# Optimization experiments

Hardware: AMD Instinct MI355X
Metric: run time of the kernel (lower is better)

The kernel has to match this reference:

```python
import jax, jax.numpy as jnp
import numpy as np

D_MODEL = 1024
N_HEADS = 16
HEAD_DIM = D_MODEL // N_HEADS


def setup_inputs() -> dict:
    key = jax.random.key(0)
    ks = jax.random.split(key, 11)
    B, S = 4, 2048
    scale = 1.0 / np.sqrt(D_MODEL)
    inp = {
        "Q": jax.random.normal(ks[0], (B, S, D_MODEL), jnp.float32),
        "K": jax.random.normal(ks[1], (B, S, D_MODEL), jnp.float32),
        "V": jax.random.normal(ks[2], (B, S, D_MODEL), jnp.float32),
        "Wq": jax.random.normal(ks[3], (D_MODEL, D_MODEL), jnp.float32) * scale,
        "bq": jnp.zeros((D_MODEL,), jnp.float32),
        "Wk": jax.random.normal(ks[4], (D_MODEL, D_MODEL), jnp.float32) * scale,
        "bk": jnp.zeros((D_MODEL,), jnp.float32),
        "Wv": jax.random.normal(ks[5], (D_MODEL, D_MODEL), jnp.float32) * scale,
        "bv": jnp.zeros((D_MODEL,), jnp.float32),
        "Wo": jax.random.normal(ks[6], (D_MODEL, D_MODEL), jnp.float32) * scale,
        "bo": jnp.zeros((D_MODEL,), jnp.float32),
    }
    return inp


def reference(Q, K, V, Wq, bq, Wk, bk, Wv, bv, Wo, bo):
    B, S, _ = Q.shape
    # Linear projections (torch nn.Linear: x @ W.T + b)
    q = Q @ Wq.T + bq
    k = K @ Wk.T + bk
    v = V @ Wv.T + bv
    # [B, S, H, Dh] -> [B, H, S, Dh]
    q = q.reshape(B, S, N_HEADS, HEAD_DIM).transpose(0, 2, 1, 3)
    k = k.reshape(B, S, N_HEADS, HEAD_DIM).transpose(0, 2, 1, 3)
    v = v.reshape(B, S, N_HEADS, HEAD_DIM).transpose(0, 2, 1, 3)
    inv_sqrt_dh = 1.0 / np.sqrt(HEAD_DIM)
    scores = jnp.einsum("bhqd,bhkd->bhqk", q, k) * inv_sqrt_dh  # [B,H,S,S]
    attn = jax.nn.softmax(scores, axis=-1)
    out = jnp.einsum("bhqk,bhkd->bhqd", attn, v)  # [B,H,S,Dh]
    out = out.transpose(0, 2, 1, 3).reshape(B, S, D_MODEL)
    return out @ Wo.T + bo
```

## Files before the change

kernel.cpp:

```cpp
#include <hip/hip_runtime.h>
#include <hip/hip_bf16.h>
#include <stdint.h>
#include <stddef.h>


typedef __bf16 bf16_t;
typedef __bf16 bf16x4 __attribute__((ext_vector_type(4)));
typedef __bf16 bf16x8 __attribute__((ext_vector_type(8)));
typedef float f32x4 __attribute__((ext_vector_type(4)));

#define D_MODEL 1024
#define M_ROWS  8192
#define S_LEN   2048
#define N_HEADS 16
#define HEAD_DIM 64
#define GBK 32
#define NT (D_MODEL / GBK)

__device__ __forceinline__ void async_copy16(void* lds, const void* g) {
    __builtin_amdgcn_global_load_lds(
        (const __attribute__((address_space(1))) void*)g,
        (__attribute__((address_space(3))) void*)lds, 16, 0, 0);
}

__global__ __launch_bounds__(256) void conv_w(
    const float* __restrict__ s0, const float* __restrict__ s1, const float* __restrict__ s2,
    bf16_t* __restrict__ d0, bf16_t* __restrict__ d1, bf16_t* __restrict__ d2)
{
    const float* s; bf16_t* d;
    if (blockIdx.y == 0)      { s = s0; d = d0; }
    else if (blockIdx.y == 1) { s = s1; d = d1; }
    else                      { s = s2; d = d2; }
    const int i = (blockIdx.x * 256 + threadIdx.x) * 8;
    const f32x4 a = *(const f32x4*)(s + i);
    const f32x4 b = *(const f32x4*)(s + i + 4);
    bf16x8 o;
#pragma unroll
    for (int j = 0; j < 4; j++) { o[j] = (bf16_t)a[j]; o[4 + j] = (bf16_t)b[j]; }
    *(bf16x8*)(d + i) = o;
}

__global__ __launch_bounds__(256, 3) void gemm_proj(
    const float* __restrict__ A0, const bf16_t* __restrict__ W0, const float* __restrict__ b0,
    const float* __restrict__ A1, const bf16_t* __restrict__ W1, const float* __restrict__ b1,
    const float* __restrict__ A2, const bf16_t* __restrict__ W2, const float* __restrict__ b2,
    bf16_t* C0, bf16_t* C1, bf16_t* C2)
{
    const int lin = blockIdx.x + ((int)blockIdx.y << 3) + ((int)blockIdx.z << 9);
    const int nl  = (lin & 7) * 192 + (lin >> 3);
    const int z   = nl >> 9;
    const int rem = nl & 511;
    const int bm0 = (rem >> 3) * 128;
    const int bn0 = (rem & 7) * 128;

    const float* A; const bf16_t* W; const float* bias; bf16_t* C;
    if (z == 0)      { A = A0; W = W0; bias = b0; C = C0; }
    else if (z == 1) { A = A1; W = W1; bias = b1; C = C1; }
    else             { A = A2; W = W2; bias = b2; C = C2; }
    const float cs = (z == 1) ? 1.4426950408889634f : 1.0f;

    __align__(16) __shared__ bf16_t sA[2][128 * 36];
    __align__(16) __shared__ bf16_t sW[2][128 * GBK];

    const int t    = threadIdx.x;
    const int lane = t & 63;
    const int w    = t >> 6;
    const int wm   = (w & 1) * 64;
    const int wn   = (w >> 1) * 64;
    const int q4   = lane >> 4;
    const int l16  = lane & 15;

    const int srow  = t >> 1;
    const int cbase = (t & 1) * 2;
    const float* aptr = &A[(size_t)(bm0 + srow) * D_MODEL + cbase * 8];

    auto stageW = [&](int buf, int kt) {
#pragma unroll
        for (int i = 0; i < 2; i++) {
            const int cid = i * 256 + t;
            const int row = cid >> 2;
            const int cg  = (cid & 3) ^ (row & 3);
            async_copy16(&sW[buf][cid * 8],
                         &W[(size_t)(bn0 + row) * D_MODEL + kt * GBK + cg * 8]);
        }
    };

    f32x4 arA[4], arB[4];
#pragma unroll
    for (int c = 0; c < 4; c++) {
        arA[c] = *(const f32x4*)(aptr + c * 4);
        arB[c] = *(const f32x4*)(aptr + GBK + c * 4);
    }
    stageW(0, 0);

    f32x4 acc[4][4];
    const f32x4 zero4 = {0.f, 0.f, 0.f, 0.f};
#pragma unroll
    for (int i = 0; i < 4; i++)
#pragma unroll
        for (int j = 0; j < 4; j++) acc[i][j] = zero4;

    auto body = [&](int kt, int buf, f32x4 (&ar)[4]) {
        bf16x8 abf[2];
#pragma unroll
        for (int c = 0; c < 4; c++)
#pragma unroll
            for (int j = 0; j < 4; j++)
                abf[c >> 1][(c & 1) * 4 + j] = (bf16_t)ar[c][j];
#pragma unroll
        for (int hb = 0; hb < 2; hb++) {
            const int slot = (cbase + hb) ^ (srow & 3);
            *(bf16x8*)&sA[buf][srow * 36 + slot * 8] = abf[hb];
        }
        __syncthreads();
        if (kt + 2 < NT) {
            const float* ap = aptr + (size_t)(kt + 2) * GBK;
#pragma unroll
            for (int c = 0; c < 4; c++) ar[c] = *(const f32x4*)(ap + c * 4);
        }
        if (kt + 1 < NT) stageW(buf ^ 1, kt + 1);

        bf16x8 af[4], bfr[4];
#pragma unroll
        for (int i = 0; i < 4; i++) {
            const int m = wm + i * 16 + l16;
            af[i]  = *(const bf16x8*)&sA[buf][m * 36 + (q4 ^ (m & 3)) * 8];
            const int n = wn + i * 16 + l16;
            bfr[i] = *(const bf16x8*)&sW[buf][n * GBK + (q4 ^ (n & 3)) * 8];
        }
#pragma unroll
        for (int i = 0; i < 4; i++)
#pragma unroll
            for (int j = 0; j < 4; j++)
                acc[i][j] = __builtin_amdgcn_mfma_f32_16x16x32_bf16(af[i], bfr[j], acc[i][j], 0, 0, 0);
    };

    for (int kt = 0; kt < NT; kt += 2) {
        body(kt,     0, arA);
        body(kt + 1, 1, arB);
    }

    if (z != 2) {
#pragma unroll
        for (int j = 0; j < 4; j++) {
            const int col = bn0 + wn + j * 16 + l16;
            const float bj = bias[col];
#pragma unroll
            for (int i = 0; i < 4; i++) {
                const int rowb = bm0 + wm + i * 16 + q4 * 4;
#pragma unroll
                for (int r = 0; r < 4; r++)
                    C[(size_t)(rowb + r) * D_MODEL + col] = (bf16_t)((acc[i][j][r] + bj) * cs);
            }
        }
    } else {
        const int bb = bm0 >> 11;
        const int sbase = (bm0 & 2047) + wm;
#pragma unroll
        for (int j = 0; j < 4; j++) {
            const int col = bn0 + wn + j * 16 + l16;
            const float bj = bias[col];
            bf16_t* ct = C + ((size_t)bb * 1024 + col) * 2048;
#pragma unroll
            for (int i = 0; i < 4; i++) {
                const int s0 = sbase + i * 16 + q4 * 4;
                const int s0p = (s0 & ~31) | (((s0 >> 2) & 3) << 3) | (((s0 >> 4) & 1) << 2);
                bf16x4 v4;
#pragma unroll
                for (int r = 0; r < 4; r++) v4[r] = (bf16_t)(acc[i][j][r] + bj);
                *(bf16x4*)&ct[s0p] = v4;
            }
        }
    }
}

__global__ __launch_bounds__(256, 3) void gemm_out(
    const bf16_t* __restrict__ A, const bf16_t* __restrict__ W,
    const float* __restrict__ bias, float* __restrict__ C)
{
    const int lin = blockIdx.x + ((int)blockIdx.y << 3);
    const int nl  = (lin & 7) * 64 + (lin >> 3);
    const int bm0 = (nl >> 3) * 128;
    const int bn0 = (nl & 7) * 128;

    __align__(16) __shared__ bf16_t sA[2][128 * GBK];
    __align__(16) __shared__ bf16_t sW[2][128 * GBK];

    const int t    = threadIdx.x;
    const int lane = t & 63;
    const int w    = t >> 6;
    const int wm   = (w & 1) * 64;
    const int wn   = (w >> 1) * 64;
    const int q4   = lane >> 4;
    const int l16  = lane & 15;

    auto stage = [&](int buf, int kt) {
#pragma unroll
        for (int i = 0; i < 2; i++) {
            const int cid = i * 256 + t;
            const int row = cid >> 2;
            const int cg  = (cid & 3) ^ (row & 3);
            async_copy16(&sA[buf][cid * 8],
                         &A[(size_t)(bm0 + row) * D_MODEL + kt * GBK + cg * 8]);
            async_copy16(&sW[buf][cid * 8],
                         &W[(size_t)(bn0 + row) * D_MODEL + kt * GBK + cg * 8]);
        }
    };

    stage(0, 0);

    f32x4 acc[4][4];
    const f32x4 zero4 = {0.f, 0.f, 0.f, 0.f};
#pragma unroll
    for (int i = 0; i < 4; i++)
#pragma unroll
        for (int j = 0; j < 4; j++) acc[i][j] = zero4;

    for (int kt = 0; kt < NT; ++kt) {
        const int buf = kt & 1;
        __syncthreads();
        if (kt + 1 < NT) stage(buf ^ 1, kt + 1);

        bf16x8 af[4], bfr[4];
#pragma unroll
        for (int i = 0; i < 4; i++) {
            const int m = wm + i * 16 + l16;
            af[i]  = *(const bf16x8*)&sA[buf][m * GBK + (q4 ^ (m & 3)) * 8];
            const int n = wn + i * 16 + l16;
            bfr[i] = *(const bf16x8*)&sW[buf][n * GBK + (q4 ^ (n & 3)) * 8];
        }
#pragma unroll
        for (int i = 0; i < 4; i++)
#pragma unroll
            for (int j = 0; j < 4; j++)
                acc[i][j] = __builtin_amdgcn_mfma_f32_16x16x32_bf16(af[i], bfr[j], acc[i][j], 0, 0, 0);
    }

#pragma unroll
    for (int j = 0; j < 4; j++) {
        const int col = bn0 + wn + j * 16 + l16;
        const float bj = bias[col];
#pragma unroll
        for (int i = 0; i < 4; i++) {
            const int rowb = bm0 + wm + i * 16 + q4 * 4;
#pragma unroll
            for (int r = 0; r < 4; r++)
                C[(size_t)(rowb + r) * D_MODEL + col] = acc[i][j][r] + bj;
        }
    }
}

#define KVT (S_LEN / 128)

__global__ __launch_bounds__(512, 3) void attn_fused(
    const bf16_t* __restrict__ q, const bf16_t* __restrict__ k,
    const bf16_t* __restrict__ vt, bf16_t* o)
{
    __align__(16) __shared__ bf16_t sK[2][128 * 64];
    __align__(16) __shared__ bf16_t sVt[2][64 * 128];

    const int t    = threadIdx.x;
    const int lane = t & 63;
    const int w    = t >> 6;
    const int head = blockIdx.x;
    const int b    = head >> 4;
    const int h    = head & 15;
    const size_t base = (size_t)b * S_LEN * D_MODEL + (size_t)h * HEAD_DIM;
    const bf16_t* vth = vt + ((size_t)b * 1024 + h * 64) * 2048;
    const int qt0  = blockIdx.y * 256;
    const int q4   = lane >> 4;
    const int l16  = lane & 15;

    bf16x8 qf[2][2];
#pragma unroll
    for (int mg = 0; mg < 2; mg++)
#pragma unroll
        for (int kk = 0; kk < 2; kk++) {
            bf16x8 tmp = *(const bf16x8*)&q[base + (size_t)(qt0 + w * 32 + mg * 16 + l16) * D_MODEL + kk * 32 + q4 * 8];
#pragma unroll
            for (int j = 0; j < 8; j++) tmp[j] = (bf16_t)((float)tmp[j] * 0.125f);
            qf[mg][kk] = tmp;
        }

    f32x4 oacc[2][4];
    const f32x4 zero4 = {0.f, 0.f, 0.f, 0.f};
#pragma unroll
    for (int mg = 0; mg < 2; mg++)
#pragma unroll
        for (int g = 0; g < 4; g++) oacc[mg][g] = zero4;
    float lsum[2] = {0.f, 0.f};

    auto stage = [&](int bf, int kt) {
        const int key0 = kt * 128;
#pragma unroll
        for (int i = 0; i < 2; i++) {
            const int cid = i * 512 + t;
            const int row = cid >> 3;
            const int cg  = (cid & 7) ^ (row & 7);
            async_copy16(&sK[bf][cid * 8], &k[base + (size_t)(key0 + row) * D_MODEL + cg * 8]);
        }
#pragma unroll
        for (int i = 0; i < 2; i++) {
            const int cid = i * 512 + t;
            const int dh  = cid >> 4;
            const int cg  = (cid & 15) ^ (dh & 15);
            async_copy16(&sVt[bf][cid * 8], &vth[(size_t)dh * 2048 + key0 + cg * 8]);
        }
    };

    stage(0, 0);
    asm volatile("s_waitcnt vmcnt(0)" ::: "memory");
    __builtin_amdgcn_s_barrier();
    __builtin_amdgcn_sched_barrier(0);

    for (int kt = 0; kt < KVT; ++kt) {
        const int cur = kt & 1;
        if (kt < KVT - 1) stage(cur ^ 1, kt + 1);

#pragma unroll
        for (int hh = 0; hh < 2; hh++) {
            f32x4 sc[2][4];
#pragma unroll
            for (int mg = 0; mg < 2; mg++)
#pragma unroll
                for (int ngl = 0; ngl < 4; ngl++) sc[mg][ngl] = zero4;
#pragma unroll
            for (int kk = 0; kk < 2; kk++)
#pragma unroll
                for (int ngl = 0; ngl < 4; ngl++) {
                    const int key = (hh * 4 + ngl) * 16 + l16;
                    const bf16x8 kf = *(const bf16x8*)&sK[cur][key * 64 + (((kk << 2) + q4) ^ (key & 7)) * 8];
#pragma unroll
                    for (int mg = 0; mg < 2; mg++)
                        sc[mg][ngl] = __builtin_amdgcn_mfma_f32_16x16x32_bf16(kf, qf[mg][kk], sc[mg][ngl], 0, 0, 0);
                }

            bf16x8 pf[2][2];
#pragma unroll
            for (int mg = 0; mg < 2; mg++) {
                float s = 0.f;
#pragma unroll
                for (int ngl = 0; ngl < 4; ngl++)
#pragma unroll
                    for (int r = 0; r < 4; r++) {
                        const float p = exp2f(sc[mg][ngl][r]);
                        sc[mg][ngl][r] = p;
                        s += p;
                    }
                lsum[mg] += s;
#pragma unroll
                for (int cl = 0; cl < 2; cl++) {
                    bf16x8 pv;
#pragma unroll
                    for (int j = 0; j < 8; j++)
                        pv[j] = (bf16_t)sc[mg][cl * 2 + (j >> 2)][j & 3];
                    pf[mg][cl] = pv;
                }
            }

#pragma unroll
            for (int cl = 0; cl < 2; cl++) {
                const int cb = (hh * 2 + cl) * 4;
#pragma unroll
                for (int g = 0; g < 4; g++) {
                    const int dh = g * 16 + l16;
                    const bf16x8 vf = *(const bf16x8*)&sVt[cur][dh * 128 + ((cb + q4) ^ l16) * 8];
#pragma unroll
                    for (int mg = 0; mg < 2; mg++)
                        oacc[mg][g] = __builtin_amdgcn_mfma_f32_16x16x32_bf16(pf[mg][cl], vf, oacc[mg][g], 0, 0, 0);
                }
            }
        }

        asm volatile("s_waitcnt vmcnt(0)" ::: "memory");
        __builtin_amdgcn_s_barrier();
        __builtin_amdgcn_sched_barrier(0);
    }

    float tsum[2];
#pragma unroll
    for (int mg = 0; mg < 2; mg++) {
        float s = lsum[mg];
        s += __shfl_xor(s, 16, 64);
        s += __shfl_xor(s, 32, 64);
        tsum[mg] = s;
    }
#pragma unroll
    for (int mg = 0; mg < 2; mg++)
#pragma unroll
        for (int r = 0; r < 4; r++) {
            const float inv = 1.0f / __shfl(tsum[mg], q4 * 4 + r, 64);
            const size_t rowoff = base + (size_t)(qt0 + w * 32 + mg * 16 + q4 * 4 + r) * D_MODEL;
#pragma unroll
            for (int g = 0; g < 4; g++)
                o[rowoff + g * 16 + l16] = (bf16_t)(oacc[mg][g][r] * inv);
        }
}

extern "C" void kernel_launch(void* const* d_in, const int* in_sizes, int n_in,
                              void* d_out, int out_size, void* d_ws, size_t ws_size,
                              hipStream_t stream) {
    const float* Q  = (const float*)d_in[0];
    const float* K  = (const float*)d_in[1];
    const float* V  = (const float*)d_in[2];
    const float* Wq = (const float*)d_in[3];
    const float* bq = (const float*)d_in[4];
    const float* Wk = (const float*)d_in[5];
    const float* bk = (const float*)d_in[6];
    const float* Wv = (const float*)d_in[7];
    const float* bv = (const float*)d_in[8];
    const float* Wo = (const float*)d_in[9];
    const float* bo = (const float*)d_in[10];
    float* out = (float*)d_out;

    bf16_t* qb  = (bf16_t*)d_ws;
    bf16_t* vb  = qb + (size_t)M_ROWS * D_MODEL;
    bf16_t* kb  = (bf16_t*)d_out;
    bf16_t* wqb = kb + (size_t)M_ROWS * D_MODEL;
    bf16_t* wkb = wqb + (size_t)D_MODEL * D_MODEL;
    bf16_t* wvb = wkb + (size_t)D_MODEL * D_MODEL;
    bf16_t* wob = vb;
    bf16_t* ob  = qb;

    conv_w<<<dim3(512, 3), dim3(256), 0, stream>>>(Wq, Wk, Wv, wqb, wkb, wvb);
    gemm_proj<<<dim3(8, 64, 3), dim3(256), 0, stream>>>(Q, wqb, bq, K, wkb, bk, V, wvb, bv, qb, kb, vb);
    attn_fused<<<dim3(4 * N_HEADS, S_LEN / 256), dim3(512), 0, stream>>>(qb, kb, vb, ob);
    conv_w<<<dim3(512, 1), dim3(256), 0, stream>>>(Wo, Wo, Wo, wob, wob, wob);
    gemm_out<<<dim3(8, 64), dim3(256), 0, stream>>>(ob, wob, bo, out);
}
```

Measured before the change: 401.2 us.

## Fold Q scale into projection, compute softmax row sums via MFMA, pack bf16 conversions

Moves the 1/sqrt(head_dim) scaling of Q into the projection GEMM epilogue so the attention kernel no longer rescales Q fragments. Replaces per-lane scalar accumulation of softmax denominators and the final shuffle reduction with an extra MFMA against a ones vector, which also uses the bf16-rounded probabilities. Converts probabilities with packed v_cvt_pk_bf16_f32 and adds s_setprio around MFMA sections. This trades VALU adds for extra matrix instructions, and the sums now come from bf16-rounded values.

```diff
diff --git a/kernel.cpp b/kernel.cpp
--- a/kernel.cpp
+++ b/kernel.cpp
@@ -21,6 +21,12 @@
     __builtin_amdgcn_global_load_lds(
         (const __attribute__((address_space(1))) void*)g,
         (__attribute__((address_space(3))) void*)lds, 16, 0, 0);
+}
+
+__device__ __forceinline__ uint32_t cvt_pk_bf16(float lo, float hi) {
+    uint32_t r;
+    asm("v_cvt_pk_bf16_f32 %0, %1, %2" : "=v"(r) : "v"(lo), "v"(hi));
+    return r;
 }
 
 __global__ __launch_bounds__(256) void conv_w(
@@ -57,7 +63,7 @@
     if (z == 0)      { A = A0; W = W0; bias = b0; C = C0; }
     else if (z == 1) { A = A1; W = W1; bias = b1; C = C1; }
     else             { A = A2; W = W2; bias = b2; C = C2; }
-    const float cs = (z == 1) ? 1.4426950408889634f : 1.0f;
+    const float cs = (z == 0) ? 0.125f : (z == 1) ? 1.4426950408889634f : 1.0f;
 
     __align__(16) __shared__ bf16_t sA[2][128 * 36];
     __align__(16) __shared__ bf16_t sW[2][128 * GBK];
@@ -275,20 +281,20 @@
 #pragma unroll
     for (int mg = 0; mg < 2; mg++)
 #pragma unroll
-        for (int kk = 0; kk < 2; kk++) {
-            bf16x8 tmp = *(const bf16x8*)&q[base + (size_t)(qt0 + w * 32 + mg * 16 + l16) * D_MODEL + kk * 32 + q4 * 8];
-#pragma unroll
-            for (int j = 0; j < 8; j++) tmp[j] = (bf16_t)((float)tmp[j] * 0.125f);
-            qf[mg][kk] = tmp;
-        }
-
+        for (int kk = 0; kk < 2; kk++)
+            qf[mg][kk] = *(const bf16x8*)&q[base + (size_t)(qt0 + w * 32 + mg * 16 + l16) * D_MODEL + kk * 32 + q4 * 8];
+
+    const f32x4 zero4 = {0.f, 0.f, 0.f, 0.f};
     f32x4 oacc[2][4];
-    const f32x4 zero4 = {0.f, 0.f, 0.f, 0.f};
 #pragma unroll
     for (int mg = 0; mg < 2; mg++)
 #pragma unroll
         for (int g = 0; g < 4; g++) oacc[mg][g] = zero4;
-    float lsum[2] = {0.f, 0.f};
+    f32x4 sacc[2] = {zero4, zero4};
+
+    bf16x8 ones;
+#pragma unroll
+    for (int j = 0; j < 8; j++) ones[j] = (bf16_t)1.0f;
 
     auto stage = [&](int bf, int kt) {
         const int key0 = kt * 128;
@@ -320,44 +326,42 @@
 #pragma unroll
         for (int hh = 0; hh < 2; hh++) {
             f32x4 sc[2][4];
-#pragma unroll
-            for (int mg = 0; mg < 2; mg++)
-#pragma unroll
-                for (int ngl = 0; ngl < 4; ngl++) sc[mg][ngl] = zero4;
-#pragma unroll
-            for (int kk = 0; kk < 2; kk++)
-#pragma unroll
-                for (int ngl = 0; ngl < 4; ngl++) {
-                    const int key = (hh * 4 + ngl) * 16 + l16;
-                    const bf16x8 kf = *(const bf16x8*)&sK[cur][key * 64 + (((kk << 2) + q4) ^ (key & 7)) * 8];
-#pragma unroll
-                    for (int mg = 0; mg < 2; mg++)
-                        sc[mg][ngl] = __builtin_amdgcn_mfma_f32_16x16x32_bf16(kf, qf[mg][kk], sc[mg][ngl], 0, 0, 0);
-                }
-
-            bf16x8 pf[2][2];
-#pragma unroll
-            for (int mg = 0; mg < 2; mg++) {
-                float s = 0.f;
-#pragma unroll
-                for (int ngl = 0; ngl < 4; ngl++)
-#pragma unroll
-                    for (int r = 0; r < 4; r++) {
-                        const float p = exp2f(sc[mg][ngl][r]);
-                        sc[mg][ngl][r] = p;
-                        s += p;
-                    }
-                lsum[mg] += s;
-#pragma unroll
-                for (int cl = 0; cl < 2; cl++) {
-                    bf16x8 pv;
-#pragma unroll
-                    for (int j = 0; j < 8; j++)
-                        pv[j] = (bf16_t)sc[mg][cl * 2 + (j >> 2)][j & 3];
-                    pf[mg][cl] = pv;
+            __builtin_amdgcn_s_setprio(1);
+#pragma unroll
+            for (int ngl = 0; ngl < 4; ngl++) {
+                const int key = (hh * 4 + ngl) * 16 + l16;
+                const bf16x8 kf0 = *(const bf16x8*)&sK[cur][key * 64 + ((q4) ^ (key & 7)) * 8];
+                const bf16x8 kf1 = *(const bf16x8*)&sK[cur][key * 64 + ((4 + q4) ^ (key & 7)) * 8];
+#pragma unroll
+                for (int mg = 0; mg < 2; mg++) {
+                    sc[mg][ngl] = __builtin_amdgcn_mfma_f32_16x16x32_bf16(kf0, qf[mg][0], zero4, 0, 0, 0);
+                    sc[mg][ngl] = __builtin_amdgcn_mfma_f32_16x16x32_bf16(kf1, qf[mg][1], sc[mg][ngl], 0, 0, 0);
                 }
             }
-
+            __builtin_amdgcn_s_setprio(0);
+
+            bf16x8 pf[2][2];
+#pragma unroll
+            for (int mg = 0; mg < 2; mg++) {
+#pragma unroll
+                for (int ngl = 0; ngl < 4; ngl++)
+#pragma unroll
+                    for (int r = 0; r < 4; r++)
+                        sc[mg][ngl][r] = exp2f(sc[mg][ngl][r]);
+#pragma unroll
+                for (int cl = 0; cl < 2; cl++) {
+                    union { uint32_t u[4]; bf16x8 v; } pk;
+#pragma unroll
+                    for (int dw = 0; dw < 4; dw++) {
+                        const int c = cl * 2 + (dw >> 1);
+                        const int e = (dw & 1) * 2;
+                        pk.u[dw] = cvt_pk_bf16(sc[mg][c][e], sc[mg][c][e + 1]);
+                    }
+                    pf[mg][cl] = pk.v;
+                }
+            }
+
+            __builtin_amdgcn_s_setprio(1);
 #pragma unroll
             for (int cl = 0; cl < 2; cl++) {
                 const int cb = (hh * 2 + cl) * 4;
@@ -369,7 +373,11 @@
                     for (int mg = 0; mg < 2; mg++)
                         oacc[mg][g] = __builtin_amdgcn_mfma_f32_16x16x32_bf16(pf[mg][cl], vf, oacc[mg][g], 0, 0, 0);
                 }
+#pragma unroll
+                for (int mg = 0; mg < 2; mg++)
+                    sacc[mg] = __builtin_amdgcn_mfma_f32_16x16x32_bf16(pf[mg][cl], ones, sacc[mg], 0, 0, 0);
             }
+            __builtin_amdgcn_s_setprio(0);
         }
 
         asm volatile("s_waitcnt vmcnt(0)" ::: "memory");
@@ -377,19 +385,11 @@
         __builtin_amdgcn_sched_barrier(0);
     }
 
-    float tsum[2];
-#pragma unroll
-    for (int mg = 0; mg < 2; mg++) {
-        float s = lsum[mg];
-        s += __shfl_xor(s, 16, 64);
-        s += __shfl_xor(s, 32, 64);
-        tsum[mg] = s;
-    }
 #pragma unroll
     for (int mg = 0; mg < 2; mg++)
 #pragma unroll
         for (int r = 0; r < 4; r++) {
-            const float inv = 1.0f / __shfl(tsum[mg], q4 * 4 + r, 64);
+            const float inv = 1.0f / sacc[mg][r];
             const size_t rowoff = base + (size_t)(qt0 + w * 32 + mg * 16 + q4 * 4 + r) * D_MODEL;
 #pragma unroll
             for (int g = 0; g < 4; g++)
```

Result: faster. 375.9 us (-6.3%).
